# Performance work log

Measured on AMD Instinct MI355X. Metric: run time of the kernel, lower is better.

## Reference

```python
import jax, jax.numpy as jnp
import numpy as np

N_NODES = 100_000
N_EDGES = 1_600_000
D_IN, D_HID, N_CLASSES = 128, 128, 40


def setup_inputs() -> dict:
    key = jax.random.key(0)
    ks = jax.random.split(key, 8)
    x = jax.random.normal(ks[0], (N_NODES, D_IN), dtype=jnp.float32)
    edge_index = jax.random.randint(ks[1], (2, N_EDGES), 0, N_NODES, dtype=jnp.int64)
    dims = [(D_IN, D_HID), (D_HID, D_HID), (D_HID, N_CLASSES)]
    inp = {"x": x, "edge_index": edge_index}
    for i, (di, do) in enumerate(dims):
        s = 1.0 / np.sqrt(di)
        inp[f"W_l{i}"] = jax.random.normal(ks[2 + 2 * i], (di, do), dtype=jnp.float32) * s
        inp[f"W_r{i}"] = jax.random.normal(ks[3 + 2 * i], (di, do), dtype=jnp.float32) * s
        inp[f"b{i}"] = jnp.zeros((do,), dtype=jnp.float32)
    return inp


def _sage_conv(x, src, dst, deg_inv, W_l, W_r, b):
    # gather messages from source nodes, mean-aggregate at target nodes
    msg = x[src]                                        # [E, d_in]
    aggr = jax.ops.segment_sum(msg, dst, num_segments=N_NODES) * deg_inv  # [N, d_in]
    return aggr @ W_l + b + x @ W_r                     # [N, d_out]


def reference(x, edge_index, W_l0, W_r0, b0, W_l1, W_r1, b1, W_l2, W_r2, b2):
    src, dst = edge_index[0], edge_index[1]
    deg = jax.ops.segment_sum(jnp.ones((N_EDGES,), x.dtype), dst, num_segments=N_NODES)
    deg_inv = (1.0 / jnp.maximum(deg, 1.0))[:, None]    # [N, 1]

    h = _sage_conv(x, src, dst, deg_inv, W_l0, W_r0, b0)
    h = jax.nn.relu(h)  # dropout p=0.3 is identity in eval mode
    h = _sage_conv(h, src, dst, deg_inv, W_l1, W_r1, b1)
    h = jax.nn.relu(h)
    h = _sage_conv(h, src, dst, deg_inv, W_l2, W_r2, b2)
    return jax.nn.log_softmax(h, axis=1)
```

## Files before the change

kernel.cpp:

```cpp
#include <hip/hip_runtime.h>
#include <math.h>

#define THREADS 256
#define BSHIFT 8
#define BSIZE 256
#define NEB 512

typedef short short8 __attribute__((ext_vector_type(8)));
typedef float f32x4 __attribute__((ext_vector_type(4)));

__device__ __forceinline__ unsigned short f2bf(float f) {
  unsigned u = __builtin_bit_cast(unsigned, f);
  return (unsigned short)((u + 0x7FFFu + ((u >> 16) & 1u)) >> 16);
}
__device__ __forceinline__ float bflo(unsigned u) {
  return __builtin_bit_cast(float, u << 16);
}
__device__ __forceinline__ float bfhi(unsigned u) {
  return __builtin_bit_cast(float, u & 0xFFFF0000u);
}
__device__ __forceinline__ unsigned pack2(float x, float y) {
  return (unsigned)f2bf(x) | ((unsigned)f2bf(y) << 16);
}


__global__ __launch_bounds__(256) void k_ehist(const int* __restrict__ dst,
                                               int* __restrict__ cnt_bm,
                                               int E, int chunk, int nbk) {
  __shared__ int h[1024];
  int blk = blockIdx.x, t = threadIdx.x;
  for (int i = t; i < nbk; i += 256) h[i] = 0;
  __syncthreads();
  int e0 = blk * chunk, e1 = min(e0 + chunk, E);
  for (int e = e0 + t; e < e1; e += 256) atomicAdd(&h[dst[e] >> BSHIFT], 1);
  __syncthreads();
  for (int i = t; i < nbk; i += 256) cnt_bm[(size_t)blk * nbk + i] = h[i];
}

__global__ __launch_bounds__(256) void k_bktscan(const int* __restrict__ cnt_bm,
                                                 int* __restrict__ locoff_tm,
                                                 int* __restrict__ bktot, int nbk) {
  int g = blockIdx.x, t = threadIdx.x;
  int c0 = cnt_bm[(size_t)(2 * t) * nbk + g];
  int c1 = cnt_bm[(size_t)(2 * t + 1) * nbk + g];
  __shared__ int sh[256];
  int s = c0 + c1;
  sh[t] = s;
  __syncthreads();
  for (int off = 1; off < 256; off <<= 1) {
    int v = (t >= off) ? sh[t - off] : 0;
    __syncthreads();
    if (t >= off) sh[t] += v;
    __syncthreads();
  }
  int excl = sh[t] - s;
  ((int2*)(locoff_tm + (size_t)g * NEB))[t] = make_int2(excl, excl + c0);
  if (t == 255) bktot[g] = sh[255];
}

__global__ __launch_bounds__(256) void k_topscan(const int* __restrict__ bktot,
                                                 int* __restrict__ bucket_base,
                                                 int nbk, int E,
                                                 int* __restrict__ row_ptr, int N) {
  __shared__ int sums[256];
  int t = threadIdx.x;
  int vals[4];
  int s = 0;
#pragma unroll
  for (int j = 0; j < 4; ++j) {
    int idx = t * 4 + j;
    vals[j] = (idx < nbk) ? bktot[idx] : 0;
    s += vals[j];
  }
  sums[t] = s;
  __syncthreads();
  for (int off = 1; off < 256; off <<= 1) {
    int v = (t >= off) ? sums[t - off] : 0;
    __syncthreads();
    if (t >= off) sums[t] += v;
    __syncthreads();
  }
  int run = sums[t] - s;
#pragma unroll
  for (int j = 0; j < 4; ++j) {
    int idx = t * 4 + j;
    if (idx < nbk) bucket_base[idx] = run;
    run += vals[j];
  }
  if (t == 0) { bucket_base[nbk] = E; row_ptr[N] = E; }
}

__global__ __launch_bounds__(256) void k_eplace(const int* __restrict__ src,
                                                const int* __restrict__ dst,
                                                const int* __restrict__ bucket_base,
                                                const int* __restrict__ locoff_tm,
                                                int* __restrict__ bedge,
                                                int E, int chunk, int nbk) {
  __shared__ int lptr[1024];
  int blk = blockIdx.x, t = threadIdx.x;
  for (int i = t; i < nbk; i += 256)
    lptr[i] = bucket_base[i] + locoff_tm[(size_t)i * NEB + blk];
  __syncthreads();
  int e0 = blk * chunk, e1 = min(e0 + chunk, E);
  for (int e = e0 + t; e < e1; e += 256) {
    int d = dst[e];
    int b = d >> BSHIFT;
    int p = atomicAdd(&lptr[b], 1);
    bedge[p] = (src[e] << 8) | (d & (BSIZE - 1));
  }
}

__global__ __launch_bounds__(256) void k_bcsr2(const int* __restrict__ bedge,
                                               const int* __restrict__ bucket_base,
                                               int* __restrict__ row_ptr,
                                               int* __restrict__ col, int N) {
  int g = blockIdx.x, t = threadIdx.x;
  int beg = bucket_base[g], end = bucket_base[g + 1];
  __shared__ int deg[BSIZE];
  __shared__ int sh[BSIZE];
  __shared__ int cur[BSIZE];
  deg[t] = 0;
  __syncthreads();
  for (int i = beg + t; i < end; i += 256)
    atomicAdd(&deg[bedge[i] & (BSIZE - 1)], 1);
  __syncthreads();
  int s = deg[t];
  sh[t] = s;
  __syncthreads();
  for (int off = 1; off < 256; off <<= 1) {
    int v = (t >= off) ? sh[t - off] : 0;
    __syncthreads();
    if (t >= off) sh[t] += v;
    __syncthreads();
  }
  int ex = beg + sh[t] - s;
  int node = g * BSIZE + t;
  if (node < N) row_ptr[node] = ex;
  cur[t] = ex;
  __syncthreads();
  for (int i = beg + t; i < end; i += 256) {
    int ed = bedge[i];
    int p = atomicAdd(&cur[ed & (BSIZE - 1)], 1);
    col[p] = ed >> 8;
  }
}

__global__ __launch_bounds__(256) void k_f2bf(const float4* __restrict__ in,
                                              ushort4* __restrict__ out, int n4) {
  int i = blockIdx.x * 256 + threadIdx.x;
  if (i < n4) {
    float4 v = in[i];
    ushort4 o;
    o.x = f2bf(v.x); o.y = f2bf(v.y); o.z = f2bf(v.z); o.w = f2bf(v.w);
    out[i] = o;
  }
}

__global__ __launch_bounds__(256) void k_wswz(const float* __restrict__ Wl,
                                              const float* __restrict__ Wr,
                                              unsigned short* __restrict__ out) {
  int idx = blockIdx.x * 256 + threadIdx.x;
  int j = idx & 7, lane = (idx >> 3) & 63, ct = (idx >> 9) & 15, ks = idx >> 13;
  int k = ks * 32 + (lane >> 4) * 8 + j;
  int c = ct * 16 + (lane & 15);
  float v = (c < 128) ? Wl[k * 128 + c] : Wr[k * 128 + (c - 128)];
  out[idx] = f2bf(v);
}

__global__ __launch_bounds__(256) void k_wswz40(const float* __restrict__ Wl,
                                                const float* __restrict__ Wr,
                                                unsigned short* __restrict__ out) {
  int idx = blockIdx.x * 256 + threadIdx.x;
  int j = idx & 7, lane = (idx >> 3) & 63;
  int tile = idx >> 9;
  int ct = tile % 5, ks = tile / 5;
  int k = ks * 32 + (lane >> 4) * 8 + j;
  int c = ct * 16 + (lane & 15);
  float v = (c < 40) ? Wl[k * 40 + c] : ((c < 80) ? Wr[k * 40 + (c - 40)] : 0.f);
  out[idx] = f2bf(v);
}

__global__ __launch_bounds__(256) void gemm128_mfma(
    const unsigned short* __restrict__ Xb, const unsigned short* __restrict__ Wswz,
    const float* __restrict__ bias,
    unsigned short* __restrict__ outL, unsigned short* __restrict__ outR, int M) {
  int wave = threadIdx.x >> 6, lane = threadIdx.x & 63;
  int quad = lane >> 4, n16 = lane & 15;
  int rowA = blockIdx.x * 128 + wave * 16 + n16;
  int rowB = rowA + 64;
  int rA = min(rowA, M - 1), rB = min(rowB, M - 1);
  bool okA = rowA < M, okB = rowB < M;

  short8 xf[4], xg[4];
  const unsigned short* xpA = Xb + (size_t)rA * 128 + quad * 8;
  const unsigned short* xpB = Xb + (size_t)rB * 128 + quad * 8;
#pragma unroll
  for (int ks = 0; ks < 4; ++ks) {
    xf[ks] = *(const short8*)(xpA + ks * 32);
    xg[ks] = *(const short8*)(xpB + ks * 32);
  }

  size_t obA = (size_t)rowA * 128, obB = (size_t)rowB * 128;
#pragma unroll 2
  for (int ct = 0; ct < 16; ++ct) {
    f32x4 accA = {0.f, 0.f, 0.f, 0.f};
    f32x4 accB = {0.f, 0.f, 0.f, 0.f};
    const unsigned short* wp = Wswz + (size_t)(ct * 64 + lane) * 8;
#pragma unroll
    for (int ks = 0; ks < 4; ++ks) {
      short8 wf = *(const short8*)(wp + ks * 8192);
      accA = __builtin_amdgcn_mfma_f32_16x16x32_bf16(wf, xf[ks], accA, 0, 0, 0);
      accB = __builtin_amdgcn_mfma_f32_16x16x32_bf16(wf, xg[ks], accB, 0, 0, 0);
    }
    int colh = (ct & 7) * 16 + quad * 4;
    if (ct < 8) {
      if (okA) {
        ushort4 o;
        o.x = f2bf(accA[0]); o.y = f2bf(accA[1]); o.z = f2bf(accA[2]); o.w = f2bf(accA[3]);
        *(ushort4*)(outL + obA + colh) = o;
      }
      if (okB) {
        ushort4 o;
        o.x = f2bf(accB[0]); o.y = f2bf(accB[1]); o.z = f2bf(accB[2]); o.w = f2bf(accB[3]);
        *(ushort4*)(outL + obB + colh) = o;
      }
    } else {
      float4 bv = *(const float4*)(bias + colh);
      if (okA) {
        ushort4 o;
        o.x = f2bf(accA[0] + bv.x); o.y = f2bf(accA[1] + bv.y);
        o.z = f2bf(accA[2] + bv.z); o.w = f2bf(accA[3] + bv.w);
        *(ushort4*)(outR + obA + colh) = o;
      }
      if (okB) {
        ushort4 o;
        o.x = f2bf(accB[0] + bv.x); o.y = f2bf(accB[1] + bv.y);
        o.z = f2bf(accB[2] + bv.z); o.w = f2bf(accB[3] + bv.w);
        *(ushort4*)(outR + obB + colh) = o;
      }
    }
  }
}

__global__ __launch_bounds__(256) void gemm40_mfma(
    const unsigned short* __restrict__ Xb, const unsigned short* __restrict__ Wswz,
    const float* __restrict__ bias,
    unsigned short* __restrict__ tlb, float* __restrict__ tr, int M) {
  int wave = threadIdx.x >> 6, lane = threadIdx.x & 63;
  int quad = lane >> 4, n16 = lane & 15;
  int row = blockIdx.x * 64 + wave * 16 + n16;
  int row_ld = min(row, M - 1);
  bool ok = row < M;

  short8 xf[4];
  const unsigned short* xp = Xb + (size_t)row_ld * 128 + quad * 8;
#pragma unroll
  for (int ks = 0; ks < 4; ++ks) xf[ks] = *(const short8*)(xp + ks * 32);

#pragma unroll
  for (int ct = 0; ct < 5; ++ct) {
    f32x4 acc = {0.f, 0.f, 0.f, 0.f};
    const unsigned short* wp = Wswz + (size_t)(ct * 64 + lane) * 8;
#pragma unroll
    for (int ks = 0; ks < 4; ++ks) {
      short8 wf = *(const short8*)(wp + (size_t)ks * 5 * 64 * 8);
      acc = __builtin_amdgcn_mfma_f32_16x16x32_bf16(wf, xf[ks], acc, 0, 0, 0);
    }
    int cglob = ct * 16 + quad * 4;
    if (!ok) continue;
    if (cglob < 40) {
      ushort4 o;
      o.x = f2bf(acc[0]); o.y = f2bf(acc[1]); o.z = f2bf(acc[2]); o.w = f2bf(acc[3]);
      *(ushort4*)(tlb + (size_t)row * 64 + cglob) = o;
    } else {
      int c = cglob - 40;
      float4 bv = *(const float4*)(bias + c);
      float4 o;
      o.x = acc[0] + bv.x; o.y = acc[1] + bv.y;
      o.z = acc[2] + bv.z; o.w = acc[3] + bv.w;
      *(float4*)(tr + (size_t)row * 40 + c) = o;
    }
  }
}

__global__ __launch_bounds__(256) void agg128b(
    const unsigned short* __restrict__ xl, const unsigned short* __restrict__ xr,
    const int* __restrict__ row_ptr, const int* __restrict__ col,
    unsigned short* __restrict__ h, int Nn) {
  int wave = threadIdx.x >> 6;
  int lane = threadIdx.x & 63;
  int pair = lane >> 5;
  int l32 = lane & 31;
  int n = blockIdx.x * 4 + wave;
  if (n >= Nn) return;
  int beg = row_ptr[n], end = row_ptr[n + 1];
  int deg = end - beg;
  const uint2* xlq = (const uint2*)xl;
  float a0x = 0.f, a0y = 0.f, a0z = 0.f, a0w = 0.f;
  float a1x = 0.f, a1y = 0.f, a1z = 0.f, a1w = 0.f;
  float a2x = 0.f, a2y = 0.f, a2z = 0.f, a2w = 0.f;
  float a3x = 0.f, a3y = 0.f, a3z = 0.f, a3w = 0.f;
  int e = beg + pair;
  for (int it = deg >> 3; it > 0; --it, e += 8) {
    uint2 u0 = xlq[(size_t)col[e]     * 32 + l32];
    uint2 u1 = xlq[(size_t)col[e + 2] * 32 + l32];
    uint2 u2 = xlq[(size_t)col[e + 4] * 32 + l32];
    uint2 u3 = xlq[(size_t)col[e + 6] * 32 + l32];
    a0x += bflo(u0.x); a0y += bfhi(u0.x); a0z += bflo(u0.y); a0w += bfhi(u0.y);
    a1x += bflo(u1.x); a1y += bfhi(u1.x); a1z += bflo(u1.y); a1w += bfhi(u1.y);
    a2x += bflo(u2.x); a2y += bfhi(u2.x); a2z += bflo(u2.y); a2w += bfhi(u2.y);
    a3x += bflo(u3.x); a3y += bfhi(u3.x); a3z += bflo(u3.y); a3w += bfhi(u3.y);
  }
  for (; e < end; e += 2) {
    uint2 u = xlq[(size_t)col[e] * 32 + l32];
    a0x += bflo(u.x); a0y += bfhi(u.x); a0z += bflo(u.y); a0w += bfhi(u.y);
  }
  float ax = (a0x + a1x) + (a2x + a3x);
  float ay = (a0y + a1y) + (a2y + a3y);
  float az = (a0z + a1z) + (a2z + a3z);
  float aw = (a0w + a1w) + (a2w + a3w);
  ax += __shfl_xor(ax, 32);
  ay += __shfl_xor(ay, 32);
  az += __shfl_xor(az, 32);
  aw += __shfl_xor(aw, 32);
  if (pair == 0) {
    float di = 1.0f / (float)max(deg, 1);
    uint2 r = ((const uint2*)xr)[(size_t)n * 32 + l32];
    float ox = fmaxf(fmaf(ax, di, bflo(r.x)), 0.f);
    float oy = fmaxf(fmaf(ay, di, bfhi(r.x)), 0.f);
    float oz = fmaxf(fmaf(az, di, bflo(r.y)), 0.f);
    float ow = fmaxf(fmaf(aw, di, bfhi(r.y)), 0.f);
    uint2 o;
    o.x = pack2(ox, oy);
    o.y = pack2(oz, ow);
    ((uint2*)h)[(size_t)n * 32 + l32] = o;
  }
}

__global__ __launch_bounds__(256) void agg40_lsm(
    const unsigned short* __restrict__ tlb, const float* __restrict__ tr,
    const int* __restrict__ row_ptr, const int* __restrict__ col,
    float* __restrict__ out, int Nn) {
  int wave = threadIdx.x >> 6;
  int lane = threadIdx.x & 63;
  int ew = lane >> 3;
  int l8 = lane & 7;
  int n = blockIdx.x * 4 + wave;
  if (n >= Nn) return;
  int beg = row_ptr[n], end = row_ptr[n + 1];
  int deg = end - beg;
  const uint4* tlq = (const uint4*)tlb;
  float a0[8], a1[8];
#pragma unroll
  for (int j = 0; j < 8; ++j) { a0[j] = 0.f; a1[j] = 0.f; }
  int e = beg + ew;
  for (int it = deg >> 4; it > 0; --it, e += 16) {
    uint4 u0 = tlq[(size_t)col[e] * 8 + l8];
    uint4 u1 = tlq[(size_t)col[e + 8] * 8 + l8];
    a0[0] += bflo(u0.x); a0[1] += bfhi(u0.x); a0[2] += bflo(u0.y); a0[3] += bfhi(u0.y);
    a0[4] += bflo(u0.z); a0[5] += bfhi(u0.z); a0[6] += bflo(u0.w); a0[7] += bfhi(u0.w);
    a1[0] += bflo(u1.x); a1[1] += bfhi(u1.x); a1[2] += bflo(u1.y); a1[3] += bfhi(u1.y);
    a1[4] += bflo(u1.z); a1[5] += bfhi(u1.z); a1[6] += bflo(u1.w); a1[7] += bfhi(u1.w);
  }
  for (; e < end; e += 8) {
    uint4 u = tlq[(size_t)col[e] * 8 + l8];
    a0[0] += bflo(u.x); a0[1] += bfhi(u.x); a0[2] += bflo(u.y); a0[3] += bfhi(u.y);
    a0[4] += bflo(u.z); a0[5] += bfhi(u.z); a0[6] += bflo(u.w); a0[7] += bfhi(u.w);
  }
  float v[8];
#pragma unroll
  for (int j = 0; j < 8; ++j) {
    float t = a0[j] + a1[j];
    t += __shfl_xor(t, 32);
    t += __shfl_xor(t, 16);
    t += __shfl_xor(t, 8);
    v[j] = t;
  }
  bool valid = l8 < 5;
  float di = 1.0f / (float)max(deg, 1);
  float4 r0 = valid ? *(const float4*)(tr + (size_t)n * 40 + 8 * l8)
                    : make_float4(0.f, 0.f, 0.f, 0.f);
  float4 r1 = valid ? *(const float4*)(tr + (size_t)n * 40 + 8 * l8 + 4)
                    : make_float4(0.f, 0.f, 0.f, 0.f);
  float rb[8] = {r0.x, r0.y, r0.z, r0.w, r1.x, r1.y, r1.z, r1.w};
  float vv[8];
#pragma unroll
  for (int j = 0; j < 8; ++j) vv[j] = valid ? fmaf(v[j], di, rb[j]) : -INFINITY;
  float m = vv[0];
#pragma unroll
  for (int j = 1; j < 8; ++j) m = fmaxf(m, vv[j]);
#pragma unroll
  for (int off = 4; off; off >>= 1) m = fmaxf(m, __shfl_xor(m, off));
  float ex = 0.f;
  if (valid) {
#pragma unroll
    for (int j = 0; j < 8; ++j) ex += expf(vv[j] - m);
  }
  float ssum = ex;
#pragma unroll
  for (int off = 4; off; off >>= 1) ssum += __shfl_xor(ssum, off);
  float lg = logf(ssum);
  if (ew == 0 && valid) {
    float4 o0, o1;
    o0.x = (vv[0] - m) - lg; o0.y = (vv[1] - m) - lg;
    o0.z = (vv[2] - m) - lg; o0.w = (vv[3] - m) - lg;
    o1.x = (vv[4] - m) - lg; o1.y = (vv[5] - m) - lg;
    o1.z = (vv[6] - m) - lg; o1.w = (vv[7] - m) - lg;
    *(float4*)(out + (size_t)n * 40 + 8 * l8) = o0;
    *(float4*)(out + (size_t)n * 40 + 8 * l8 + 4) = o1;
  }
}


extern "C" void kernel_launch(void* const* d_in, const int* in_sizes, int n_in,
                              void* d_out, int out_size, void* d_ws, size_t ws_size,
                              hipStream_t stream) {
  const float* x   = (const float*)d_in[0];
  const int*   ei  = (const int*)d_in[1];
  const float* Wl0 = (const float*)d_in[2];
  const float* Wr0 = (const float*)d_in[3];
  const float* b0  = (const float*)d_in[4];
  const float* Wl1 = (const float*)d_in[5];
  const float* Wr1 = (const float*)d_in[6];
  const float* b1  = (const float*)d_in[7];
  const float* Wl2 = (const float*)d_in[8];
  const float* Wr2 = (const float*)d_in[9];
  const float* b2  = (const float*)d_in[10];

  int N = in_sizes[0] / 128;
  int E = in_sizes[1] / 2;
  const int* src = ei;
  const int* dst = ei + E;
  int nbk = (N + BSIZE - 1) / BSIZE;
  int chunk = (E + NEB - 1) / NEB;

  char* ws = (char*)d_ws;
  size_t off = 0;
  auto alloc = [&](size_t bytes) -> void* {
    void* p = ws + off;
    off += (bytes + 255) & ~(size_t)255;
    return p;
  };
  unsigned short* xb  = (unsigned short*)alloc((size_t)N * 128 * 2);
  unsigned short* gA  = (unsigned short*)alloc((size_t)N * 128 * 2);
  unsigned short* gB  = (unsigned short*)alloc((size_t)N * 128 * 2);
  unsigned short* hC  = (unsigned short*)alloc((size_t)N * 128 * 2);
  unsigned short* tlb = (unsigned short*)alloc((size_t)N * 64 * 2);
  float* tr           = (float*)alloc((size_t)N * 40 * 4);
  int* row_ptr  = (int*)alloc((size_t)(N + 1) * 4);
  int* col      = (int*)alloc((size_t)E * 4);
  int* bedge    = (int*)alloc((size_t)E * 4);
  int* cnt_bm   = (int*)alloc((size_t)NEB * nbk * 4);
  int* locoff   = (int*)alloc((size_t)nbk * NEB * 4);
  int* bktot    = (int*)alloc((size_t)nbk * 4);
  int* bbase    = (int*)alloc((size_t)(nbk + 1) * 4);
  unsigned short* wswz0 = (unsigned short*)alloc(32768 * 2);
  unsigned short* wswz1 = (unsigned short*)alloc(32768 * 2);
  unsigned short* wswz2 = (unsigned short*)alloc(10240 * 2);
  (void)ws_size; (void)n_in; (void)out_size;

  k_ehist<<<NEB, 256, 0, stream>>>(dst, cnt_bm, E, chunk, nbk);
  k_bktscan<<<nbk, 256, 0, stream>>>(cnt_bm, locoff, bktot, nbk);
  k_topscan<<<1, 256, 0, stream>>>(bktot, bbase, nbk, E, row_ptr, N);
  k_eplace<<<NEB, 256, 0, stream>>>(src, dst, bbase, locoff, bedge, E, chunk, nbk);
  k_bcsr2<<<nbk, 256, 0, stream>>>(bedge, bbase, row_ptr, col, N);

  int n4 = N * 32;
  k_f2bf<<<(n4 + 255) / 256, 256, 0, stream>>>((const float4*)x, (ushort4*)xb, n4);
  k_wswz<<<128, 256, 0, stream>>>(Wl0, Wr0, wswz0);
  k_wswz<<<128, 256, 0, stream>>>(Wl1, Wr1, wswz1);
  k_wswz40<<<40, 256, 0, stream>>>(Wl2, Wr2, wswz2);

  int gg128 = (N + 127) / 128;
  int gg = (N + 63) / 64;
  int nb = (N + 3) / 4;

  gemm128_mfma<<<gg128, 256, 0, stream>>>(xb, wswz0, b0, gA, gB, N);
  agg128b<<<nb, 256, 0, stream>>>(gA, gB, row_ptr, col, hC, N);
  gemm128_mfma<<<gg128, 256, 0, stream>>>(hC, wswz1, b1, gA, gB, N);
  agg128b<<<nb, 256, 0, stream>>>(gA, gB, row_ptr, col, hC, N);
  gemm40_mfma<<<gg, 256, 0, stream>>>(hC, wswz2, b2, tlb, tr, N);
  agg40_lsm<<<nb, 256, 0, stream>>>(tlb, tr, row_ptr, col, (float*)d_out, N);
}
```

Baseline: 472.0 us.

## Fuse input bf16 conversion into first GEMM, merge weight swizzles, prefetch agg40 indices

Result: faster. 446.7 us (-5.4%).

```diff
diff --git a/kernel.cpp b/kernel.cpp
--- a/kernel.cpp
+++ b/kernel.cpp
@@ -21,6 +21,13 @@
 }
 __device__ __forceinline__ unsigned pack2(float x, float y) {
   return (unsigned)f2bf(x) | ((unsigned)f2bf(y) << 16);
+}
+
+__device__ __forceinline__ void acc8(float* a, uint4 u) {
+  a[0] += bflo(u.x); a[1] += bfhi(u.x);
+  a[2] += bflo(u.y); a[3] += bfhi(u.y);
+  a[4] += bflo(u.z); a[5] += bfhi(u.z);
+  a[6] += bflo(u.w); a[7] += bfhi(u.w);
 }
 
 
@@ -145,39 +152,108 @@
   }
 }
 
-__global__ __launch_bounds__(256) void k_f2bf(const float4* __restrict__ in,
-                                              ushort4* __restrict__ out, int n4) {
-  int i = blockIdx.x * 256 + threadIdx.x;
-  if (i < n4) {
-    float4 v = in[i];
-    ushort4 o;
-    o.x = f2bf(v.x); o.y = f2bf(v.y); o.z = f2bf(v.z); o.w = f2bf(v.w);
-    out[i] = o;
-  }
-}
-
-__global__ __launch_bounds__(256) void k_wswz(const float* __restrict__ Wl,
-                                              const float* __restrict__ Wr,
-                                              unsigned short* __restrict__ out) {
-  int idx = blockIdx.x * 256 + threadIdx.x;
-  int j = idx & 7, lane = (idx >> 3) & 63, ct = (idx >> 9) & 15, ks = idx >> 13;
-  int k = ks * 32 + (lane >> 4) * 8 + j;
-  int c = ct * 16 + (lane & 15);
-  float v = (c < 128) ? Wl[k * 128 + c] : Wr[k * 128 + (c - 128)];
-  out[idx] = f2bf(v);
-}
-
-__global__ __launch_bounds__(256) void k_wswz40(const float* __restrict__ Wl,
-                                                const float* __restrict__ Wr,
-                                                unsigned short* __restrict__ out) {
-  int idx = blockIdx.x * 256 + threadIdx.x;
-  int j = idx & 7, lane = (idx >> 3) & 63;
-  int tile = idx >> 9;
-  int ct = tile % 5, ks = tile / 5;
-  int k = ks * 32 + (lane >> 4) * 8 + j;
-  int c = ct * 16 + (lane & 15);
-  float v = (c < 40) ? Wl[k * 40 + c] : ((c < 80) ? Wr[k * 40 + (c - 40)] : 0.f);
-  out[idx] = f2bf(v);
+__global__ __launch_bounds__(256) void k_wswz_all(
+    const float* __restrict__ Wl0, const float* __restrict__ Wr0,
+    const float* __restrict__ Wl1, const float* __restrict__ Wr1,
+    const float* __restrict__ Wl2, const float* __restrict__ Wr2,
+    unsigned short* __restrict__ out0, unsigned short* __restrict__ out1,
+    unsigned short* __restrict__ out2) {
+  int b = blockIdx.x, t = threadIdx.x;
+  if (b < 256) {
+    const float* Wl = (b < 128) ? Wl0 : Wl1;
+    const float* Wr = (b < 128) ? Wr0 : Wr1;
+    unsigned short* out = (b < 128) ? out0 : out1;
+    int idx = (b & 127) * 256 + t;
+    int j = idx & 7, lane = (idx >> 3) & 63, ct = (idx >> 9) & 15, ks = idx >> 13;
+    int k = ks * 32 + (lane >> 4) * 8 + j;
+    int c = ct * 16 + (lane & 15);
+    float v = (c < 128) ? Wl[k * 128 + c] : Wr[k * 128 + (c - 128)];
+    out[idx] = f2bf(v);
+  } else {
+    int idx = (b - 256) * 256 + t;
+    int j = idx & 7, lane = (idx >> 3) & 63;
+    int tile = idx >> 9;
+    int ct = tile % 5, ks = tile / 5;
+    int k = ks * 32 + (lane >> 4) * 8 + j;
+    int c = ct * 16 + (lane & 15);
+    float v = (c < 40) ? Wl2[k * 40 + c] : ((c < 80) ? Wr2[k * 40 + (c - 40)] : 0.f);
+    out2[idx] = f2bf(v);
+  }
+}
+
+__global__ __launch_bounds__(256) void gemm128_mfma_x32(
+    const float* __restrict__ X, const unsigned short* __restrict__ Wswz,
+    const float* __restrict__ bias,
+    unsigned short* __restrict__ outL, unsigned short* __restrict__ outR, int M) {
+  int wave = threadIdx.x >> 6, lane = threadIdx.x & 63;
+  int quad = lane >> 4, n16 = lane & 15;
+  int rowA = blockIdx.x * 128 + wave * 16 + n16;
+  int rowB = rowA + 64;
+  int rA = min(rowA, M - 1), rB = min(rowB, M - 1);
+  bool okA = rowA < M, okB = rowB < M;
+
+  short8 xf[4], xg[4];
+  const float* xpA = X + (size_t)rA * 128 + quad * 8;
+  const float* xpB = X + (size_t)rB * 128 + quad * 8;
+#pragma unroll
+  for (int ks = 0; ks < 4; ++ks) {
+    float4 a0 = *(const float4*)(xpA + ks * 32);
+    float4 a1 = *(const float4*)(xpA + ks * 32 + 4);
+    float4 b0 = *(const float4*)(xpB + ks * 32);
+    float4 b1 = *(const float4*)(xpB + ks * 32 + 4);
+    short8 f, g;
+    f[0] = (short)f2bf(a0.x); f[1] = (short)f2bf(a0.y);
+    f[2] = (short)f2bf(a0.z); f[3] = (short)f2bf(a0.w);
+    f[4] = (short)f2bf(a1.x); f[5] = (short)f2bf(a1.y);
+    f[6] = (short)f2bf(a1.z); f[7] = (short)f2bf(a1.w);
+    g[0] = (short)f2bf(b0.x); g[1] = (short)f2bf(b0.y);
+    g[2] = (short)f2bf(b0.z); g[3] = (short)f2bf(b0.w);
+    g[4] = (short)f2bf(b1.x); g[5] = (short)f2bf(b1.y);
+    g[6] = (short)f2bf(b1.z); g[7] = (short)f2bf(b1.w);
+    xf[ks] = f;
+    xg[ks] = g;
+  }
+
+  size_t obA = (size_t)rowA * 128, obB = (size_t)rowB * 128;
+#pragma unroll 2
+  for (int ct = 0; ct < 16; ++ct) {
+    f32x4 accA = {0.f, 0.f, 0.f, 0.f};
+    f32x4 accB = {0.f, 0.f, 0.f, 0.f};
+    const unsigned short* wp = Wswz + (size_t)(ct * 64 + lane) * 8;
+#pragma unroll
+    for (int ks = 0; ks < 4; ++ks) {
+      short8 wf = *(const short8*)(wp + ks * 8192);
+      accA = __builtin_amdgcn_mfma_f32_16x16x32_bf16(wf, xf[ks], accA, 0, 0, 0);
+      accB = __builtin_amdgcn_mfma_f32_16x16x32_bf16(wf, xg[ks], accB, 0, 0, 0);
+    }
+    int colh = (ct & 7) * 16 + quad * 4;
+    if (ct < 8) {
+      if (okA) {
+        ushort4 o;
+        o.x = f2bf(accA[0]); o.y = f2bf(accA[1]); o.z = f2bf(accA[2]); o.w = f2bf(accA[3]);
+        *(ushort4*)(outL + obA + colh) = o;
+      }
+      if (okB) {
+        ushort4 o;
+        o.x = f2bf(accB[0]); o.y = f2bf(accB[1]); o.z = f2bf(accB[2]); o.w = f2bf(accB[3]);
+        *(ushort4*)(outL + obB + colh) = o;
+      }
+    } else {
+      float4 bv = *(const float4*)(bias + colh);
+      if (okA) {
+        ushort4 o;
+        o.x = f2bf(accA[0] + bv.x); o.y = f2bf(accA[1] + bv.y);
+        o.z = f2bf(accA[2] + bv.z); o.w = f2bf(accA[3] + bv.w);
+        *(ushort4*)(outR + obA + colh) = o;
+      }
+      if (okB) {
+        ushort4 o;
+        o.x = f2bf(accB[0] + bv.x); o.y = f2bf(accB[1] + bv.y);
+        o.z = f2bf(accB[2] + bv.z); o.w = f2bf(accB[3] + bv.w);
+        *(ushort4*)(outR + obB + colh) = o;
+      }
+    }
+  }
 }
 
 __global__ __launch_bounds__(256) void gemm128_mfma(
@@ -353,19 +429,27 @@
   float a0[8], a1[8];
 #pragma unroll
   for (int j = 0; j < 8; ++j) { a0[j] = 0.f; a1[j] = 0.f; }
-  int e = beg + ew;
-  for (int it = deg >> 4; it > 0; --it, e += 16) {
-    uint4 u0 = tlq[(size_t)col[e] * 8 + l8];
-    uint4 u1 = tlq[(size_t)col[e + 8] * 8 + l8];
-    a0[0] += bflo(u0.x); a0[1] += bfhi(u0.x); a0[2] += bflo(u0.y); a0[3] += bfhi(u0.y);
-    a0[4] += bflo(u0.z); a0[5] += bfhi(u0.z); a0[6] += bflo(u0.w); a0[7] += bfhi(u0.w);
-    a1[0] += bflo(u1.x); a1[1] += bfhi(u1.x); a1[2] += bflo(u1.y); a1[3] += bfhi(u1.y);
-    a1[4] += bflo(u1.z); a1[5] += bfhi(u1.z); a1[6] += bflo(u1.w); a1[7] += bfhi(u1.w);
-  }
-  for (; e < end; e += 8) {
-    uint4 u = tlq[(size_t)col[e] * 8 + l8];
-    a0[0] += bflo(u.x); a0[1] += bfhi(u.x); a0[2] += bflo(u.y); a0[3] += bfhi(u.y);
-    a0[4] += bflo(u.z); a0[5] += bfhi(u.z); a0[6] += bflo(u.w); a0[7] += bfhi(u.w);
+  int rounds = (deg + 15) >> 4;
+  if (rounds > 0) {
+    int end1 = end - 1;
+    int e = beg + ew;
+    int c0 = col[min(e, end1)];
+    int c1 = col[min(e + 8, end1)];
+    for (int it = rounds - 1; it > 0; --it) {
+      uint4 u0 = tlq[(size_t)c0 * 8 + l8];
+      uint4 u1 = tlq[(size_t)c1 * 8 + l8];
+      int en = e + 16;
+      int cn0 = col[min(en, end1)];
+      int cn1 = col[min(en + 8, end1)];
+      acc8(a0, u0); acc8(a1, u1);
+      c0 = cn0; c1 = cn1; e = en;
+    }
+    uint4 u0 = tlq[(size_t)c0 * 8 + l8];
+    uint4 u1 = tlq[(size_t)c1 * 8 + l8];
+    uint4 z = make_uint4(0u, 0u, 0u, 0u);
+    if (e >= end) u0 = z;
+    if (e + 8 >= end) u1 = z;
+    acc8(a0, u0); acc8(a1, u1);
   }
   float v[8];
 #pragma unroll
@@ -441,7 +525,6 @@
     off += (bytes + 255) & ~(size_t)255;
     return p;
   };
-  unsigned short* xb  = (unsigned short*)alloc((size_t)N * 128 * 2);
   unsigned short* gA  = (unsigned short*)alloc((size_t)N * 128 * 2);
   unsigned short* gB  = (unsigned short*)alloc((size_t)N * 128 * 2);
   unsigned short* hC  = (unsigned short*)alloc((size_t)N * 128 * 2);
@@ -465,17 +548,14 @@
   k_eplace<<<NEB, 256, 0, stream>>>(src, dst, bbase, locoff, bedge, E, chunk, nbk);
   k_bcsr2<<<nbk, 256, 0, stream>>>(bedge, bbase, row_ptr, col, N);
 
-  int n4 = N * 32;
-  k_f2bf<<<(n4 + 255) / 256, 256, 0, stream>>>((const float4*)x, (ushort4*)xb, n4);
-  k_wswz<<<128, 256, 0, stream>>>(Wl0, Wr0, wswz0);
-  k_wswz<<<128, 256, 0, stream>>>(Wl1, Wr1, wswz1);
-  k_wswz40<<<40, 256, 0, stream>>>(Wl2, Wr2, wswz2);
+  k_wswz_all<<<296, 256, 0, stream>>>(Wl0, Wr0, Wl1, Wr1, Wl2, Wr2,
+                                      wswz0, wswz1, wswz2);
 
   int gg128 = (N + 127) / 128;
   int gg = (N + 63) / 64;
   int nb = (N + 3) / 4;
 
-  gemm128_mfma<<<gg128, 256, 0, stream>>>(xb, wswz0, b0, gA, gB, N);
+  gemm128_mfma_x32<<<gg128, 256, 0, stream>>>(x, wswz0, b0, gA, gB, N);
   agg128b<<<nb, 256, 0, stream>>>(gA, gB, row_ptr, col, hC, N);
   gemm128_mfma<<<gg128, 256, 0, stream>>>(hC, wswz1, b1, gA, gB, N);
   agg128b<<<nb, 256, 0, stream>>>(gA, gB, row_ptr, col, hC, N);
```
